# Kernel tuning notes

Hardware: AMD Instinct MI355X
Metric: run time of the kernel (lower is better)

Reference implementation:

```python
import jax, jax.numpy as jnp
import numpy as np

NUM_M = 512
NUM_T = 64
MAX_STEPS = 20
TAU = 1.0


def setup_inputs() -> dict:
    key = jax.random.key(0)
    ks = jax.random.split(key, 10)
    num_m, num_t = NUM_M, NUM_T
    inp = {
        "v_src": jax.random.normal(ks[0], (1, num_m), jnp.float32),
        "v_target": jax.random.normal(ks[1], (1, num_m), jnp.float32),
        # small-magnitude generators so matrix_exp stays well-conditioned
        "omegas": jax.random.normal(ks[2], (num_t, num_m, num_m), jnp.float32) * 0.01,
        "W1": jax.random.normal(ks[3], (2 * num_m, 256), jnp.float32) * (1.0 / np.sqrt(2 * num_m)),
        "b1": jnp.zeros((256,), jnp.float32),
        "W2": jax.random.normal(ks[4], (256, 128), jnp.float32) * (1.0 / np.sqrt(256)),
        "b2": jnp.zeros((128,), jnp.float32),
        "W3": jax.random.normal(ks[5], (128, num_t), jnp.float32) * (1.0 / np.sqrt(128)),
        "b3": jnp.zeros((num_t,), jnp.float32),
        # pre-sampled gumbel noise, one draw per step: [max_steps, B, num_t]
        "gumbel_noise": jax.random.gumbel(ks[6], (MAX_STEPS, 1, num_t), jnp.float32),
    }
    return inp


def reference(v_src, v_target, omegas, W1, b1, W2, b2, W3, b3, gumbel_noise):
    tgt_idx = jnp.argmax(v_target, axis=-1)  # [B]

    def mlp(x):
        h = jax.nn.relu(x @ W1 + b1)
        h = jax.nn.relu(h @ W2 + b2)
        return h @ W3 + b3  # [B, num_t]

    batched_expm = jax.vmap(jax.scipy.linalg.expm)

    def step(carry, g):
        v, done = carry  # v: [B, num_m], done: [B] bool
        x = jnp.concatenate([v, v_target], axis=-1)        # [B, 2*num_m]
        logits = mlp(x)                                     # [B, num_t]
        # gumbel_softmax(tau=1.0, hard=False)
        soft = jax.nn.softmax((logits + g) / TAU, axis=-1)
        omega_k = jnp.einsum('bt,tmk->bmk', soft, omegas)   # [B, m, m]
        R_k = batched_expm(omega_k)                         # [B, m, m]
        v_new = jnp.einsum('bmk,bk->bm', R_k, v)            # [B, m]
        # freeze state and zero-pad logits once the target marking was reached
        v_out = jnp.where(done[:, None], v, v_new)
        logits_out = jnp.where(done[:, None], jnp.zeros_like(logits), logits)
        done_new = done | (jnp.argmax(v_new, axis=-1) == tgt_idx)
        return (v_out, done_new), logits_out

    done0 = jnp.zeros((v_src.shape[0],), bool)
    (v_final, _), logits_seq = jax.lax.scan(step, (v_src, done0), gumbel_noise)
    # logits_seq: [max_steps, B, num_t]; B==1 -> [max_steps, num_t] (torch squeeze(0))
    return v_final, logits_seq[:, 0, :]
```

## Files before the change

### kernel.cpp

```cpp
#include <hip/hip_runtime.h>
#include <hip/hip_fp16.h>


#define NBLK 256
#define NTHR 512
#define NSTEP 20
#define NTAY 3
#define RBUF 4

typedef unsigned long long ull;

#define XW(buf, i) (X + ((((buf) << 8) + (i)) << 3))

__device__ __forceinline__ float wredsum(float p) {
#pragma unroll
  for (int off = 32; off > 0; off >>= 1) p += __shfl_xor(p, off, 64);
  return p;
}

__device__ __forceinline__ void wredsum2(float& p0, float& p1) {
#pragma unroll
  for (int off = 32; off > 0; off >>= 1) {
    float t0 = __shfl_xor(p0, off, 64);
    float t1 = __shfl_xor(p1, off, 64);
    p0 += t0;
    p1 += t1;
  }
}

__device__ __forceinline__ void publish2(ull* w, float v0, float v1, unsigned int tag2) {
  unsigned int u0 = (__float_as_uint(v0) & ~3u) | tag2;
  ull x = (ull)u0 | ((ull)__float_as_uint(v1) << 32);
  __hip_atomic_store(w, x, __ATOMIC_RELAXED, __HIP_MEMORY_SCOPE_AGENT);
}

__device__ __forceinline__ float2 poll2(ull* w, unsigned int tag2) {
  int it = 0;
  for (;;) {
    ull x = __hip_atomic_load(w, __ATOMIC_RELAXED, __HIP_MEMORY_SCOPE_AGENT);
    if ((unsigned int)(x & 3u) == tag2) {
      float2 r;
      r.x = __uint_as_float((unsigned int)x);
      r.y = __uint_as_float((unsigned int)(x >> 32));
      return r;
    }
    if (it == 0)      __builtin_amdgcn_s_sleep(1);
    else if (it == 1) __builtin_amdgcn_s_sleep(2);
    else              __builtin_amdgcn_s_sleep(4);
    if (it < 2) ++it;
  }
}

__device__ __forceinline__ void poll8(ull* w0, unsigned int tg, float* o) {
  ull x0 = 0, x1 = 0, x2 = 0, x3 = 0;
  bool g0 = false, g1 = false, g2 = false, g3 = false;
  int it = 0;
  for (;;) {
    if (!g0) { ull x = __hip_atomic_load(w0,      __ATOMIC_RELAXED, __HIP_MEMORY_SCOPE_AGENT); if ((unsigned int)(x & 3u) == tg) { x0 = x; g0 = true; } }
    if (!g1) { ull x = __hip_atomic_load(w0 + 8,  __ATOMIC_RELAXED, __HIP_MEMORY_SCOPE_AGENT); if ((unsigned int)(x & 3u) == tg) { x1 = x; g1 = true; } }
    if (!g2) { ull x = __hip_atomic_load(w0 + 16, __ATOMIC_RELAXED, __HIP_MEMORY_SCOPE_AGENT); if ((unsigned int)(x & 3u) == tg) { x2 = x; g2 = true; } }
    if (!g3) { ull x = __hip_atomic_load(w0 + 24, __ATOMIC_RELAXED, __HIP_MEMORY_SCOPE_AGENT); if ((unsigned int)(x & 3u) == tg) { x3 = x; g3 = true; } }
    if (g0 && g1 && g2 && g3) break;
    if (it == 0)      __builtin_amdgcn_s_sleep(1);
    else if (it == 1) __builtin_amdgcn_s_sleep(2);
    else              __builtin_amdgcn_s_sleep(4);
    if (it < 2) ++it;
  }
  o[0] = __uint_as_float((unsigned int)x0); o[1] = __uint_as_float((unsigned int)(x0 >> 32));
  o[2] = __uint_as_float((unsigned int)x1); o[3] = __uint_as_float((unsigned int)(x1 >> 32));
  o[4] = __uint_as_float((unsigned int)x2); o[5] = __uint_as_float((unsigned int)(x2 >> 32));
  o[6] = __uint_as_float((unsigned int)x3); o[7] = __uint_as_float((unsigned int)(x3 >> 32));
}

__global__ __launch_bounds__(NTHR) void petri_kernel(
    const float* __restrict__ vsrc, const float* __restrict__ vtgt,
    const float* __restrict__ omg,  const float* __restrict__ W1,
    const float* __restrict__ b1,   const float* __restrict__ W2,
    const float* __restrict__ b2,   const float* __restrict__ W3,
    const float* __restrict__ b3,   const float* __restrict__ gum,
    ull* __restrict__ X, float* __restrict__ out) {
  __shared__ __half2 oh[64 * 512];
  __shared__ __align__(16) float A0_s[512];
  __shared__ __align__(16) float A1_s[512];
  __shared__ __align__(16) float v_loc[512];
  __shared__ float tgt_s[512];
  __shared__ float w1c_s[1024];
  __shared__ float gum_s[NSTEP * 64];
  __shared__ float b2_s[128], b3_s[64];
  __shared__ float soft_s[64], h1_s[256], h2_s[128];
  __shared__ float redp[512];
  __shared__ float llog[NSTEP * 64];
  __shared__ float rf8[8];
  __shared__ int   ri8[8];
  __shared__ float cB_s[1];
  __shared__ int   bc[1];

  const int b = blockIdx.x, tid = threadIdx.x;
  const int wv = tid >> 6, ln = tid & 63;

  v_loc[tid] = vsrc[tid];
  tgt_s[tid] = vtgt[tid];
  w1c_s[tid] = W1[tid * 256 + b];
  w1c_s[tid + 512] = W1[(tid + 512) * 256 + b];
  for (int i = tid; i < NSTEP * 64; i += NTHR) gum_s[i] = gum[i];
  if (tid >= NTHR - 128) {
    int j = tid - (NTHR - 128);
    b2_s[j] = b2[j];
    if (j < 64) b3_s[j] = b3[j];
  }
  float w2r[64];
  {
    const int o = tid & 127, q = tid >> 7;
    const float* p = W2 + ((q << 6) * 128) + o;
#pragma unroll
    for (int i = 0; i < 64; ++i) w2r[i] = p[i * 128];
  }
  float w3r[16];
  {
    const int o = tid & 63, q = tid >> 6;
    const float* p = W3 + ((q << 4) * 64) + o;
#pragma unroll
    for (int i = 0; i < 16; ++i) w3r[i] = p[i * 64];
  }
  {
    const int tq = tid >> 7;
    const int c4 = (tid & 127) << 2;
    const float* rp = omg + (b << 10) + c4;
#pragma unroll 4
    for (int g = 0; g < 16; ++g) {
      const int t = (g << 2) + tq;
      const float* p = rp + t * 262144;
      const float4 f0 = *(const float4*)(p);
      const float4 f1 = *(const float4*)(p + 512);
      __half2* dst = oh + t * 512 + c4;
      dst[0] = __floats2half2_rn(f0.x, f1.x);
      dst[1] = __floats2half2_rn(f0.y, f1.y);
      dst[2] = __floats2half2_rn(f0.z, f1.z);
      dst[3] = __floats2half2_rn(f0.w, f1.w);
    }
  }
  __syncthreads();

  {
    float p = tgt_s[tid] * w1c_s[tid + 512];
    p = wredsum(p);
    if (ln == 0) rf8[wv] = p;
    __syncthreads();
    if (tid == 0) {
      float a = b1[b];
      for (int q = 0; q < 8; ++q) a += rf8[q];
      cB_s[0] = a;
    }
    __syncthreads();
  }

  int tgtIdx;
  {
    float v = tgt_s[tid]; int ix = tid;
#pragma unroll
    for (int off = 32; off > 0; off >>= 1) {
      float ov = __shfl_xor(v, off, 64); int oi = __shfl_xor(ix, off, 64);
      if (ov > v || (ov == v && oi < ix)) { v = ov; ix = oi; }
    }
    if (ln == 0) { rf8[wv] = v; ri8[wv] = ix; }
    __syncthreads();
    if (tid == 0) {
      float bv = rf8[0]; int bix = ri8[0];
      for (int q = 1; q < 8; ++q)
        if (rf8[q] > bv || (rf8[q] == bv && ri8[q] < bix)) { bv = rf8[q]; bix = ri8[q]; }
      bc[0] = bix;
    }
    __syncthreads();
    tgtIdx = bc[0];
    __syncthreads();
  }

  float vreg[8], w1t[8];
  if (wv == 0) {
    const int l8 = ln << 3;
#pragma unroll
    for (int k = 0; k < 8; ++k) { vreg[k] = v_loc[l8 + k]; w1t[k] = w1c_s[l8 + k]; }
    float p = 0.f;
#pragma unroll
    for (int k = 0; k < 8; ++k) p = fmaf(vreg[k], w1t[k], p);
    p = wredsum(p);
    if (ln == 0) {
      float h = fmaxf(p + cB_s[0], 0.f);
      publish2(XW(0, b), h, h, 0u);
    }
  }

  int d = 0;
  int nAct = 0;
  int r = 0;

  for (int s = 0; s < NSTEP; ++s) {
    if (d) continue;
    nAct = s + 1;

    {
      const int buf = r & (RBUF - 1);
      const unsigned int tg = (unsigned int)((r >> 2) & 3);
      if (tid < 256) h1_s[tid] = poll2(XW(buf, tid), tg).x;
      __syncthreads();
      ++r;
    }

    {
      const int q = tid >> 7;
      const float* hp = h1_s + (q << 6);
      float a0 = 0.f, a1 = 0.f, a2 = 0.f, a3 = 0.f;
#pragma unroll
      for (int i = 0; i < 64; i += 4) {
        a0 = fmaf(hp[i],     w2r[i],     a0);
        a1 = fmaf(hp[i + 1], w2r[i + 1], a1);
        a2 = fmaf(hp[i + 2], w2r[i + 2], a2);
        a3 = fmaf(hp[i + 3], w2r[i + 3], a3);
      }
      redp[tid] = (a0 + a1) + (a2 + a3);
    }
    __syncthreads();
    if (tid < 128) {
      float rr = redp[tid] + redp[tid + 128] + redp[tid + 256] + redp[tid + 384] + b2_s[tid];
      h2_s[tid] = fmaxf(rr, 0.f);
    }
    __syncthreads();
    {
      const int q = tid >> 6;
      const float* hp = h2_s + (q << 4);
      float a0 = 0.f, a1 = 0.f;
#pragma unroll
      for (int i = 0; i < 16; i += 2) {
        a0 = fmaf(hp[i],     w3r[i],     a0);
        a1 = fmaf(hp[i + 1], w3r[i + 1], a1);
      }
      redp[tid] = a0 + a1;
    }
    __syncthreads();
    if (tid < 64) {
      float a = b3_s[tid];
#pragma unroll
      for (int q = 0; q < 8; ++q) a += redp[tid + (q << 6)];
      float lg = a + gum_s[s * 64 + tid];
      float mx = lg;
#pragma unroll
      for (int off = 32; off > 0; off >>= 1) mx = fmaxf(mx, __shfl_xor(mx, off, 64));
      float e = __expf(lg - mx);
      float sm = e;
#pragma unroll
      for (int off = 32; off > 0; off >>= 1) sm += __shfl_xor(sm, off, 64);
      soft_s[tid] = e / sm;
      llog[s * 64 + tid] = a;
    }
    __syncthreads();

    {
      float a0 = 0.f, a1 = 0.f, c0 = 0.f, c1 = 0.f;
#pragma unroll 8
      for (int t = 0; t < 64; t += 2) {
        float2 xy0 = __half22float2(oh[t * 512 + tid]);
        float2 xy1 = __half22float2(oh[(t + 1) * 512 + tid]);
        float s0 = soft_s[t], s1 = soft_s[t + 1];
        a0 = fmaf(s0, xy0.x, a0);
        c0 = fmaf(s0, xy0.y, c0);
        a1 = fmaf(s1, xy1.x, a1);
        c1 = fmaf(s1, xy1.y, c1);
      }
      A0_s[tid] = a0 + a1;
      A1_s[tid] = c0 + c1;
    }
    __syncthreads();

    if (wv == 0) {
      const int l8 = ln << 3;
      const float4 a00 = *(const float4*)(A0_s + l8);
      const float4 a01 = *(const float4*)(A0_s + l8 + 4);
      const float4 a10 = *(const float4*)(A1_s + l8);
      const float4 a11 = *(const float4*)(A1_s + l8 + 4);
      const float vb0 = v_loc[b << 1], vb1 = v_loc[(b << 1) + 1];
      float wreg[8];
#pragma unroll
      for (int k = 0; k < 8; ++k) wreg[k] = vreg[k];
      float acc0 = 0.f, acc1 = 0.f;
#pragma unroll
      for (int n = 1; n <= NTAY; ++n) {
        const int rr = r + (n - 1);
        const int buf = rr & (RBUF - 1);
        const unsigned int tg = (unsigned int)((rr >> 2) & 3);
        float p0 = 0.f, p1 = 0.f;
        p0 = fmaf(a00.x, wreg[0], p0); p0 = fmaf(a00.y, wreg[1], p0);
        p0 = fmaf(a00.z, wreg[2], p0); p0 = fmaf(a00.w, wreg[3], p0);
        p0 = fmaf(a01.x, wreg[4], p0); p0 = fmaf(a01.y, wreg[5], p0);
        p0 = fmaf(a01.z, wreg[6], p0); p0 = fmaf(a01.w, wreg[7], p0);
        p1 = fmaf(a10.x, wreg[0], p1); p1 = fmaf(a10.y, wreg[1], p1);
        p1 = fmaf(a10.z, wreg[2], p1); p1 = fmaf(a10.w, wreg[3], p1);
        p1 = fmaf(a11.x, wreg[4], p1); p1 = fmaf(a11.y, wreg[5], p1);
        p1 = fmaf(a11.z, wreg[6], p1); p1 = fmaf(a11.w, wreg[7], p1);
        wredsum2(p0, p1);
        if (ln == 0) {
          float s0, s1;
          if (n == 1) {
            s0 = p0; s1 = p1;
            acc0 = vb0 + s0; acc1 = vb1 + s1;
          } else {
            const float inv = (n == 2) ? 0.5f : (1.0f / 3.0f);
            s0 = p0 * inv; s1 = p1 * inv;
            acc0 += s0; acc1 += s1;
          }
          const float q0 = (n < NTAY) ? s0 : acc0;
          const float q1 = (n < NTAY) ? s1 : acc1;
          publish2(XW(buf, b), q0, q1, tg);
        }
        poll8(XW(buf, (ln << 2)), tg, wreg);
      }
      if (s + 1 < NSTEP) {
        const int rh = r + NTAY;
        const unsigned int tgh = (unsigned int)((rh >> 2) & 3);
        float ph = 0.f;
#pragma unroll
        for (int k = 0; k < 8; ++k) ph = fmaf(wreg[k], w1t[k], ph);
        ph = wredsum(ph);
        if (ln == 0) {
          float h = fmaxf(ph + cB_s[0], 0.f);
          publish2(XW(rh & (RBUF - 1), b), h, h, tgh);
        }
      }
#pragma unroll
      for (int k = 0; k < 8; ++k) vreg[k] = wreg[k];
      *(float4*)(v_loc + l8)     = make_float4(wreg[0], wreg[1], wreg[2], wreg[3]);
      *(float4*)(v_loc + l8 + 4) = make_float4(wreg[4], wreg[5], wreg[6], wreg[7]);
      float mv = wreg[0]; int mi = l8;
#pragma unroll
      for (int k = 1; k < 8; ++k) if (wreg[k] > mv) { mv = wreg[k]; mi = l8 + k; }
#pragma unroll
      for (int off = 32; off > 0; off >>= 1) {
        float ov = __shfl_xor(mv, off, 64); int oi = __shfl_xor(mi, off, 64);
        if (ov > mv || (ov == mv && oi < mi)) { mv = ov; mi = oi; }
      }
      if (ln == 0) bc[0] = (mi == tgtIdx) ? 1 : 0;
    }
    __syncthreads();
    if (bc[0]) d = 1;
    r += NTAY;
  }

  if (b == 0) {
    out[tid] = v_loc[tid];
    for (int i = tid; i < NSTEP * 64; i += NTHR)
      out[512 + i] = (i < nAct * 64) ? llog[i] : 0.0f;
  }
}

extern "C" void kernel_launch(void* const* d_in, const int* in_sizes, int n_in,
                              void* d_out, int out_size, void* d_ws, size_t ws_size,
                              hipStream_t stream) {
  (void)in_sizes; (void)n_in; (void)out_size; (void)ws_size;
  petri_kernel<<<dim3(NBLK), dim3(NTHR), 0, stream>>>(
      (const float*)d_in[0], (const float*)d_in[1], (const float*)d_in[2],
      (const float*)d_in[3], (const float*)d_in[4], (const float*)d_in[5],
      (const float*)d_in[6], (const float*)d_in[7], (const float*)d_in[8],
      (const float*)d_in[9], (ull*)d_ws, (float*)d_out);
}
```

Before: 320.0 us.

## Fuse MLP layer-2 reduction into layer-3 and overlap h1 polling with expm

Computes the h2 relu values on the fly inside the layer-3 dot product, which removes one barrier and the h2_s staging buffer; a second reduction buffer keeps redp intact while this happens. The next step's h1 gather is now done by waves 1-4 while wave 0 runs the Taylor/expm exchange, so the poll at the top of each step disappears. The ring buffer is replaced by fixed slots with a step-parity tag. This adds redundant layer-2 reduction work per thread and busy-polling waves that sleep, and the fixed-slot tag scheme is a possible correctness risk if blocks drift apart by several steps.

Result: slower. 348.7 us (+9.0%).

```diff
diff --git a/kernel.cpp b/kernel.cpp
--- a/kernel.cpp
+++ b/kernel.cpp
@@ -87,8 +87,9 @@
   __shared__ float w1c_s[1024];
   __shared__ float gum_s[NSTEP * 64];
   __shared__ float b2_s[128], b3_s[64];
-  __shared__ float soft_s[64], h1_s[256], h2_s[128];
+  __shared__ float soft_s[64], h1_s[256];
   __shared__ float redp[512];
+  __shared__ float redq[512];
   __shared__ float llog[NSTEP * 64];
   __shared__ float rf8[8];
   __shared__ int   ri8[8];
@@ -189,22 +190,16 @@
       publish2(XW(0, b), h, h, 0u);
     }
   }
+  if (tid < 256) h1_s[tid] = poll2(XW(0, tid), 0u).x;
+  __syncthreads();
 
   int d = 0;
   int nAct = 0;
-  int r = 0;
 
   for (int s = 0; s < NSTEP; ++s) {
     if (d) continue;
     nAct = s + 1;
-
-    {
-      const int buf = r & (RBUF - 1);
-      const unsigned int tg = (unsigned int)((r >> 2) & 3);
-      if (tid < 256) h1_s[tid] = poll2(XW(buf, tid), tg).x;
-      __syncthreads();
-      ++r;
-    }
+    const unsigned int tgS = (unsigned int)(s & 3);
 
     {
       const int q = tid >> 7;
@@ -220,27 +215,27 @@
       redp[tid] = (a0 + a1) + (a2 + a3);
     }
     __syncthreads();
-    if (tid < 128) {
-      float rr = redp[tid] + redp[tid + 128] + redp[tid + 256] + redp[tid + 384] + b2_s[tid];
-      h2_s[tid] = fmaxf(rr, 0.f);
-    }
-    __syncthreads();
+
     {
-      const int q = tid >> 6;
-      const float* hp = h2_s + (q << 4);
+      const int q3 = wv;
+      const int base = q3 << 4;
       float a0 = 0.f, a1 = 0.f;
 #pragma unroll
-      for (int i = 0; i < 16; i += 2) {
-        a0 = fmaf(hp[i],     w3r[i],     a0);
-        a1 = fmaf(hp[i + 1], w3r[i + 1], a1);
-      }
-      redp[tid] = a0 + a1;
-    }
-    __syncthreads();
+      for (int k = 0; k < 16; k += 2) {
+        const int i0 = base + k, i1 = base + k + 1;
+        const float h20 = fmaxf(redp[i0] + redp[i0 + 128] + redp[i0 + 256] + redp[i0 + 384] + b2_s[i0], 0.f);
+        const float h21 = fmaxf(redp[i1] + redp[i1 + 128] + redp[i1 + 256] + redp[i1 + 384] + b2_s[i1], 0.f);
+        a0 = fmaf(h20, w3r[k],     a0);
+        a1 = fmaf(h21, w3r[k + 1], a1);
+      }
+      redq[tid] = a0 + a1;
+    }
+    __syncthreads();
+
     if (tid < 64) {
       float a = b3_s[tid];
 #pragma unroll
-      for (int q = 0; q < 8; ++q) a += redp[tid + (q << 6)];
+      for (int q = 0; q < 8; ++q) a += redq[tid + (q << 6)];
       float lg = a + gum_s[s * 64 + tid];
       float mx = lg;
 #pragma unroll
@@ -284,9 +279,6 @@
       float acc0 = 0.f, acc1 = 0.f;
 #pragma unroll
       for (int n = 1; n <= NTAY; ++n) {
-        const int rr = r + (n - 1);
-        const int buf = rr & (RBUF - 1);
-        const unsigned int tg = (unsigned int)((rr >> 2) & 3);
         float p0 = 0.f, p1 = 0.f;
         p0 = fmaf(a00.x, wreg[0], p0); p0 = fmaf(a00.y, wreg[1], p0);
         p0 = fmaf(a00.z, wreg[2], p0); p0 = fmaf(a00.w, wreg[3], p0);
@@ -309,20 +301,18 @@
           }
           const float q0 = (n < NTAY) ? s0 : acc0;
           const float q1 = (n < NTAY) ? s1 : acc1;
-          publish2(XW(buf, b), q0, q1, tg);
+          publish2(XW(n, b), q0, q1, tgS);
         }
-        poll8(XW(buf, (ln << 2)), tg, wreg);
+        poll8(XW(n, (ln << 2)), tgS, wreg);
       }
       if (s + 1 < NSTEP) {
-        const int rh = r + NTAY;
-        const unsigned int tgh = (unsigned int)((rh >> 2) & 3);
         float ph = 0.f;
 #pragma unroll
         for (int k = 0; k < 8; ++k) ph = fmaf(wreg[k], w1t[k], ph);
         ph = wredsum(ph);
         if (ln == 0) {
           float h = fmaxf(ph + cB_s[0], 0.f);
-          publish2(XW(rh & (RBUF - 1), b), h, h, tgh);
+          publish2(XW(0, b), h, h, (unsigned int)((s + 1) & 3));
         }
       }
 #pragma unroll
@@ -338,10 +328,24 @@
         if (ov > mv || (ov == mv && oi < mi)) { mv = ov; mi = oi; }
       }
       if (ln == 0) bc[0] = (mi == tgtIdx) ? 1 : 0;
+    } else if (wv <= 4) {
+      if (s + 1 < NSTEP) {
+        const int w = tid - 64;
+        ull* addr = XW(0, w);
+        const unsigned int tgh = (unsigned int)((s + 1) & 3);
+        __builtin_amdgcn_s_sleep(64);
+        for (;;) {
+          ull x = __hip_atomic_load(addr, __ATOMIC_RELAXED, __HIP_MEMORY_SCOPE_AGENT);
+          if ((unsigned int)(x & 3u) == tgh) {
+            h1_s[w] = __uint_as_float((unsigned int)x);
+            break;
+          }
+          __builtin_amdgcn_s_sleep(8);
+        }
+      }
     }
     __syncthreads();
     if (bc[0]) d = 1;
-    r += NTAY;
   }
 
   if (b == 0) {
```
